# Optimization experiments

Measured on AMD Instinct MI355X. Metric: run time of the kernel, lower is better.

## Reference

```python
import jax, jax.numpy as jnp
import numpy as np

N_NODES = 100000
N_EDGES = 1600000
D_IN = 64
D_HID = 64
D_MLP = 32
D_OUT = 1


def setup_inputs() -> dict:
    key = jax.random.key(0)
    ks = jax.random.split(key, 12)
    s_in = 1.0 / np.sqrt(D_IN)
    s_h = 1.0 / np.sqrt(D_HID)
    s_m = 1.0 / np.sqrt(D_MLP)
    return {
        "x": jax.random.normal(ks[0], (N_NODES, D_IN), dtype=jnp.float32),
        "edge_index": jax.random.randint(ks[1], (2, N_EDGES), 0, N_NODES, dtype=jnp.int32),
        # SAGEConv 1: lin_l (aggregated neighbors, with bias), lin_r (root, no bias)
        "W1l": jax.random.normal(ks[2], (D_IN, D_HID), dtype=jnp.float32) * s_in,
        "b1l": jnp.zeros((D_HID,), dtype=jnp.float32),
        "W1r": jax.random.normal(ks[3], (D_IN, D_HID), dtype=jnp.float32) * s_in,
        # SAGEConv 2
        "W2l": jax.random.normal(ks[4], (D_HID, D_HID), dtype=jnp.float32) * s_h,
        "b2l": jnp.zeros((D_HID,), dtype=jnp.float32),
        "W2r": jax.random.normal(ks[5], (D_HID, D_HID), dtype=jnp.float32) * s_h,
        # MLP head
        "Wf1": jax.random.normal(ks[6], (D_HID, D_MLP), dtype=jnp.float32) * s_h,
        "bf1": jnp.zeros((D_MLP,), dtype=jnp.float32),
        "Wf2": jax.random.normal(ks[7], (D_MLP, D_OUT), dtype=jnp.float32) * s_m,
        "bf2": jnp.zeros((D_OUT,), dtype=jnp.float32),
    }


def _sage_conv(h, src, dst, Wl, bl, Wr):
    # mean-aggregate neighbor features (messages flow src -> dst)
    n = h.shape[0]
    agg = jax.ops.segment_sum(h[src], dst, num_segments=n)  # [N, D]
    cnt = jax.ops.segment_sum(jnp.ones((src.shape[0], 1), h.dtype), dst, num_segments=n)
    mean = agg / jnp.maximum(cnt, 1.0)  # isolated nodes -> 0
    return mean @ Wl + bl + h @ Wr


def reference(x, edge_index, W1l, b1l, W1r, W2l, b2l, W2r, Wf1, bf1, Wf2, bf2):
    src, dst = edge_index[0], edge_index[1]
    h = jax.nn.relu(_sage_conv(x, src, dst, W1l, b1l, W1r))
    h = jax.nn.relu(_sage_conv(h, src, dst, W2l, b2l, W2r))
    h = jax.nn.relu(h @ Wf1 + bf1)
    return jax.nn.sigmoid(h @ Wf2 + bf2)  # [N, 1]
```

## Files before the change

kernel.cpp:

```cpp
#include <hip/hip_runtime.h>
#include <math.h>

#define NN 100000
#define NE 1600000
#define D 64
#define DM 32
#define BK 128
#define NBUCK ((NN + BK - 1) / BK)
#define CAP 2560
#define MS_CHUNK 4096
#define N_MS ((NE + MS_CHUNK - 1) / MS_CHUNK)
#define NTILE ((NN + 63) / 64)

typedef unsigned int uint32;
typedef unsigned short ushort16;
typedef __attribute__((ext_vector_type(8))) short short8v;
typedef __attribute__((ext_vector_type(4))) float float4v;
typedef __attribute__((ext_vector_type(4))) uint32 uint4v;

__device__ __forceinline__ ushort16 f2bf(float f) {
    unsigned u = __float_as_uint(f);
    unsigned r = (u + 0x7FFF + ((u >> 16) & 1)) >> 16;
    return (ushort16)r;
}
__device__ __forceinline__ float bfLo(uint32 u) { return __uint_as_float(u << 16); }
__device__ __forceinline__ float bfHi(uint32 u) { return __uint_as_float(u & 0xFFFF0000u); }

__global__ __launch_bounds__(256) void prep_kernel(
    const float4* __restrict__ xin, ushort4* __restrict__ xoutb, int n4,
    const float* __restrict__ W1l, const float* __restrict__ W1r,
    const float* __restrict__ W2l, const float* __restrict__ W2r,
    const float* __restrict__ Wf1,
    ushort16* __restrict__ bfragL1, ushort16* __restrict__ bfragL2,
    ushort16* __restrict__ b2frag,
    int* __restrict__ bucketCursor)
{
    int b = blockIdx.x;
    if (b < 1024) {
        for (int i = b * 256 + threadIdx.x; i < n4; i += 1024 * 256) {
            float4 v = xin[i];
            ushort4 o;
            o.x = f2bf(v.x); o.y = f2bf(v.y); o.z = f2bf(v.z); o.w = f2bf(v.w);
            xoutb[i] = o;
        }
    } else if (b < 1056) {
        int tid = (b - 1024) * 256 + threadIdx.x;
        {
            int idx = tid;
            int i = idx & 7, l = (idx >> 3) & 63, jt = (idx >> 9) & 3, kb = idx >> 11;
            int k = kb * 32 + (l >> 4) * 8 + i;
            int j = jt * 16 + (l & 15);
            float v1 = (k < 64) ? W1l[k * 64 + j] : W1r[(k - 64) * 64 + j];
            float v2 = (k < 64) ? W2l[k * 64 + j] : W2r[(k - 64) * 64 + j];
            bfragL1[idx] = f2bf(v1);
            bfragL2[idx] = f2bf(v2);
        }
        if (tid < 2048) {
            int idx = tid;
            int i = idx & 7, l = (idx >> 3) & 63, jt2 = (idx >> 9) & 1, kb2 = idx >> 10;
            int k = kb2 * 32 + (l >> 4) * 8 + i;
            int j = jt2 * 16 + (l & 15);
            b2frag[idx] = f2bf(Wf1[k * 32 + j]);
        }
    } else {
        for (int t = threadIdx.x; t < NBUCK; t += 256)
            bucketCursor[t] = t * CAP;
    }
}

__global__ __launch_bounds__(1024) void multisplit_kernel(
    const int* __restrict__ src, const int* __restrict__ dst,
    int* __restrict__ bucketCursor, uint32* __restrict__ edgesPacked)
{
    __shared__ int lh[NBUCK];
    __shared__ int lbase[NBUCK];
    int t = threadIdx.x;
    if (t < NBUCK) lh[t] = 0;
    __syncthreads();
    int base = blockIdx.x * MS_CHUNK;
#pragma unroll
    for (int i = 0; i < MS_CHUNK / 1024; ++i) {
        int e = base + i * 1024 + t;
        if (e < NE) atomicAdd(&lh[dst[e] >> 7], 1);
    }
    __syncthreads();
    if (t < NBUCK) {
        int c = lh[t];
        lbase[t] = c ? atomicAdd(&bucketCursor[t], c) : 0;
        lh[t] = 0;
    }
    __syncthreads();
#pragma unroll
    for (int i = 0; i < MS_CHUNK / 1024; ++i) {
        int e = base + i * 1024 + t;
        if (e < NE) {
            int d = dst[e];
            int b = d >> 7;
            int r = atomicAdd(&lh[b], 1);
            edgesPacked[lbase[b] + r] = ((uint32)src[e] << 7) | (uint32)(d & 127);
        }
    }
}

__global__ __launch_bounds__(256) void reorder_csr_kernel(
    const uint32* __restrict__ edgesPacked,
    const int* __restrict__ bucketEnd,
    int* __restrict__ rowBeg, int* __restrict__ deg,
    int* __restrict__ sortedSrc)
{
    __shared__ int lcnt[BK];
    __shared__ int sc[BK];
    __shared__ int rowBegL[BK];
    int t = threadIdx.x;
    int b = blockIdx.x;
    int eBeg = b * CAP, eEnd = bucketEnd[b];

    if (t < BK) lcnt[t] = 0;
    __syncthreads();
    for (int e = eBeg + t; e < eEnd; e += 256)
        atomicAdd(&lcnt[edgesPacked[e] & 127], 1);
    __syncthreads();

    int myCnt = (t < BK) ? lcnt[t] : 0;
    if (t < BK) sc[t] = myCnt;
    __syncthreads();
#pragma unroll
    for (int off = 1; off < BK; off <<= 1) {
        int v = 0;
        if (t < BK && t >= off) v = sc[t - off];
        __syncthreads();
        if (t < BK) sc[t] += v;
        __syncthreads();
    }
    if (t < BK) {
        int excl = sc[t] - myCnt;
        int begHere = eBeg + excl;
        rowBegL[t] = begHere;
        int node = b * BK + t;
        if (node < NN) {
            rowBeg[node] = begHere;
            deg[node] = myCnt;
        }
        lcnt[t] = 0;
    }
    __syncthreads();

    for (int e = eBeg + t; e < eEnd; e += 256) {
        uint32 u = edgesPacked[e];
        int rel = (int)(u & 127);
        int rank = atomicAdd(&lcnt[rel], 1);
        sortedSrc[rowBegL[rel] + rank] = (int)(u >> 7);
    }
}

__global__ __launch_bounds__(256) void gather_mean_kernel(
    const uint2* __restrict__ hb2,
    const int* __restrict__ rowBeg, const int* __restrict__ deg,
    const int* __restrict__ ss,
    uint2* __restrict__ meanb2,
    int n)
{
    int lane = threadIdx.x & 63;
    int wid = threadIdx.x >> 6;
    int q = lane & 15;
    int g = lane >> 4;

    for (int node = blockIdx.x * 4 + wid; node < n; node += gridDim.x * 4) {
        int dg = deg[node];
        const int* ep = ss + rowBeg[node];
        float a0 = 0.f, a1 = 0.f, a2 = 0.f, a3 = 0.f;
        int nq = dg >> 2;
        int i = 0;
        for (; i + 4 <= nq; i += 4) {
            int s0 = ep[(i + 0) * 4 + g];
            int s1 = ep[(i + 1) * 4 + g];
            int s2 = ep[(i + 2) * 4 + g];
            int s3 = ep[(i + 3) * 4 + g];
            uint2 u0 = hb2[(size_t)s0 * 16 + q];
            uint2 u1 = hb2[(size_t)s1 * 16 + q];
            uint2 u2 = hb2[(size_t)s2 * 16 + q];
            uint2 u3 = hb2[(size_t)s3 * 16 + q];
            a0 += (bfLo(u0.x) + bfLo(u1.x)) + (bfLo(u2.x) + bfLo(u3.x));
            a1 += (bfHi(u0.x) + bfHi(u1.x)) + (bfHi(u2.x) + bfHi(u3.x));
            a2 += (bfLo(u0.y) + bfLo(u1.y)) + (bfLo(u2.y) + bfLo(u3.y));
            a3 += (bfHi(u0.y) + bfHi(u1.y)) + (bfHi(u2.y) + bfHi(u3.y));
        }
        for (; i < nq; ++i) {
            int s = ep[i * 4 + g];
            uint2 u = hb2[(size_t)s * 16 + q];
            a0 += bfLo(u.x); a1 += bfHi(u.x);
            a2 += bfLo(u.y); a3 += bfHi(u.y);
        }
        int rem = dg & 3;
        if (rem && g < rem) {
            int s = ep[nq * 4 + g];
            uint2 u = hb2[(size_t)s * 16 + q];
            a0 += bfLo(u.x); a1 += bfHi(u.x);
            a2 += bfLo(u.y); a3 += bfHi(u.y);
        }
        a0 += __shfl_xor(a0, 16); a0 += __shfl_xor(a0, 32);
        a1 += __shfl_xor(a1, 16); a1 += __shfl_xor(a1, 32);
        a2 += __shfl_xor(a2, 16); a2 += __shfl_xor(a2, 32);
        a3 += __shfl_xor(a3, 16); a3 += __shfl_xor(a3, 32);
        if (lane < 16) {
            float inv = (dg > 0) ? 1.0f / (float)dg : 0.0f;
            uint2 o;
            o.x = (uint32)f2bf(a0 * inv) | ((uint32)f2bf(a1 * inv) << 16);
            o.y = (uint32)f2bf(a2 * inv) | ((uint32)f2bf(a3 * inv) << 16);
            meanb2[(size_t)node * 16 + q] = o;
        }
    }
}

template <int WITH_MLP>
__global__ __launch_bounds__(256) void sage_mfma_kernel(
    const ushort16* __restrict__ rootb,
    const uint32* __restrict__ meanb32,
    const ushort16* __restrict__ bfrag,
    const ushort16* __restrict__ b2frag,
    const float* __restrict__ bl,
    const float* __restrict__ bf1, const float* __restrict__ Wf2,
    const float* __restrict__ bf2,
    ushort16* __restrict__ houtb,
    float* __restrict__ outp,
    int n)
{
    __shared__ ushort16 h2L[WITH_MLP ? (64 * 64) : 1];

    int lane = threadIdx.x & 63;
    int w = threadIdx.x >> 6;
    int c = lane & 15;
    int g = lane >> 4;
    int blkBase = blockIdx.x * 64;

    int arow = blkBase + w * 16 + c;
    bool aval = (arow < n);
    uint4v zero4 = {0u, 0u, 0u, 0u};
    const uint32* mrow = meanb32 + (size_t)arow * 32;
    const uint32* xrow = (const uint32*)rootb + (size_t)arow * 32;
    uint4v am0 = aval ? *(const uint4v*)(mrow + g * 4) : zero4;
    uint4v am1 = aval ? *(const uint4v*)(mrow + 16 + g * 4) : zero4;
    uint4v ax0 = aval ? *(const uint4v*)(xrow + g * 4) : zero4;
    uint4v ax1 = aval ? *(const uint4v*)(xrow + 16 + g * 4) : zero4;
    short8v a0 = __builtin_bit_cast(short8v, am0);
    short8v a1 = __builtin_bit_cast(short8v, am1);
    short8v a2 = __builtin_bit_cast(short8v, ax0);
    short8v a3 = __builtin_bit_cast(short8v, ax1);

    const short8v* bf = (const short8v*)bfrag;
    float4v acc[4];
#pragma unroll
    for (int jt = 0; jt < 4; ++jt) acc[jt] = (float4v){0.f, 0.f, 0.f, 0.f};
#pragma unroll
    for (int jt = 0; jt < 4; ++jt) {
        acc[jt] = __builtin_amdgcn_mfma_f32_16x16x32_bf16(a0, bf[(0 * 4 + jt) * 64 + lane], acc[jt], 0, 0, 0);
        acc[jt] = __builtin_amdgcn_mfma_f32_16x16x32_bf16(a1, bf[(1 * 4 + jt) * 64 + lane], acc[jt], 0, 0, 0);
        acc[jt] = __builtin_amdgcn_mfma_f32_16x16x32_bf16(a2, bf[(2 * 4 + jt) * 64 + lane], acc[jt], 0, 0, 0);
        acc[jt] = __builtin_amdgcn_mfma_f32_16x16x32_bf16(a3, bf[(3 * 4 + jt) * 64 + lane], acc[jt], 0, 0, 0);
    }

    float blv[4];
#pragma unroll
    for (int jt = 0; jt < 4; ++jt) blv[jt] = bl[jt * 16 + c];

    if (!WITH_MLP) {
#pragma unroll
        for (int jt = 0; jt < 4; ++jt) {
#pragma unroll
            for (int r = 0; r < 4; ++r) {
                int nd = blkBase + w * 16 + g * 4 + r;
                if (nd < n)
                    houtb[(size_t)nd * 64 + jt * 16 + c] =
                        f2bf(fmaxf(acc[jt][r] + blv[jt], 0.0f));
            }
        }
    } else {
#pragma unroll
        for (int jt = 0; jt < 4; ++jt) {
            int j = jt * 16 + c;
#pragma unroll
            for (int r = 0; r < 4; ++r) {
                int row = w * 16 + g * 4 + r;
                ushort16 hv = f2bf(fmaxf(acc[jt][r] + blv[jt], 0.0f));
                h2L[row * 64 + (((j >> 3) ^ (row & 7)) << 3) + (j & 7)] = hv;
            }
        }
        __syncthreads();

        int arow2 = w * 16 + c;
        short8v a2f[2];
#pragma unroll
        for (int kb2 = 0; kb2 < 2; ++kb2) {
            int chunk = (kb2 * 4 + g) ^ (arow2 & 7);
            a2f[kb2] = *(const short8v*)&h2L[arow2 * 64 + chunk * 8];
        }
        const short8v* b2f = (const short8v*)b2frag;
        float4v acc2[2];
#pragma unroll
        for (int jt2 = 0; jt2 < 2; ++jt2) acc2[jt2] = (float4v){0.f, 0.f, 0.f, 0.f};
#pragma unroll
        for (int jt2 = 0; jt2 < 2; ++jt2) {
            acc2[jt2] = __builtin_amdgcn_mfma_f32_16x16x32_bf16(a2f[0], b2f[(0 * 2 + jt2) * 64 + lane], acc2[jt2], 0, 0, 0);
            acc2[jt2] = __builtin_amdgcn_mfma_f32_16x16x32_bf16(a2f[1], b2f[(1 * 2 + jt2) * 64 + lane], acc2[jt2], 0, 0, 0);
        }

        float bf1v[2], f2v[2];
#pragma unroll
        for (int jt2 = 0; jt2 < 2; ++jt2) {
            bf1v[jt2] = bf1[jt2 * 16 + c];
            f2v[jt2]  = Wf2[jt2 * 16 + c];
        }
        float bias2 = bf2[0];

        float pv[4];
#pragma unroll
        for (int r = 0; r < 4; ++r) {
            float t = 0.0f;
#pragma unroll
            for (int jt2 = 0; jt2 < 2; ++jt2) {
                float h3 = fmaxf(acc2[jt2][r] + bf1v[jt2], 0.0f);
                t += h3 * f2v[jt2];
            }
#pragma unroll
            for (int off = 1; off <= 8; off <<= 1) t += __shfl_xor(t, off);
            pv[r] = t;
        }
        if (c == 0) {
#pragma unroll
            for (int r = 0; r < 4; ++r) {
                int nd = blkBase + w * 16 + g * 4 + r;
                if (nd < n)
                    outp[nd] = 1.0f / (1.0f + expf(-(pv[r] + bias2)));
            }
        }
    }
}

extern "C" void kernel_launch(void* const* d_in, const int* in_sizes, int n_in,
                              void* d_out, int out_size, void* d_ws, size_t ws_size,
                              hipStream_t stream)
{
    const float* x   = (const float*)d_in[0];
    const int*   ei  = (const int*)d_in[1];
    const float* W1l = (const float*)d_in[2];
    const float* b1l = (const float*)d_in[3];
    const float* W1r = (const float*)d_in[4];
    const float* W2l = (const float*)d_in[5];
    const float* b2l = (const float*)d_in[6];
    const float* W2r = (const float*)d_in[7];
    const float* Wf1 = (const float*)d_in[8];
    const float* bf1 = (const float*)d_in[9];
    const float* Wf2 = (const float*)d_in[10];
    const float* bf2 = (const float*)d_in[11];
    float* out = (float*)d_out;

    const int* src = ei;
    const int* dst = ei + NE;

    char* ws = (char*)d_ws;
    size_t off = 0;
    auto alloc = [&](size_t bytes) {
        char* p = ws + off;
        off = (off + bytes + 255) & ~(size_t)255;
        return p;
    };
    int* bucketCursor = (int*)alloc((size_t)NBUCK * sizeof(int));
    int* rowBeg       = (int*)alloc((size_t)NN * sizeof(int));
    int* deg          = (int*)alloc((size_t)NN * sizeof(int));
    uint32* edgesPacked = (uint32*)alloc((size_t)NBUCK * CAP * sizeof(uint32));
    int* sortedSrc      = (int*)alloc((size_t)NBUCK * CAP * sizeof(int));
    ushort16* xb    = (ushort16*)alloc((size_t)NN * D * sizeof(ushort16));
    ushort16* h1b   = (ushort16*)alloc((size_t)NN * D * sizeof(ushort16));
    uint32*   meanb = (uint32*)alloc((size_t)NN * (D / 2) * sizeof(uint32));
    ushort16* bfragL1 = (ushort16*)alloc(8192 * sizeof(ushort16));
    ushort16* bfragL2 = (ushort16*)alloc(8192 * sizeof(ushort16));
    ushort16* b2frag  = (ushort16*)alloc(2048 * sizeof(ushort16));

    dim3 blk(256);

    prep_kernel<<<1057, blk, 0, stream>>>(
        (const float4*)x, (ushort4*)xb, NN * D / 4,
        W1l, W1r, W2l, W2r, Wf1, bfragL1, bfragL2, b2frag, bucketCursor);

    multisplit_kernel<<<N_MS, dim3(1024), 0, stream>>>(src, dst, bucketCursor, edgesPacked);
    reorder_csr_kernel<<<NBUCK, blk, 0, stream>>>(
        edgesPacked, bucketCursor, rowBeg, deg, sortedSrc);

    gather_mean_kernel<<<2048, blk, 0, stream>>>(
        (const uint2*)xb, rowBeg, deg, sortedSrc, (uint2*)meanb, NN);
    sage_mfma_kernel<0><<<NTILE, blk, 0, stream>>>(
        xb, meanb, bfragL1, b2frag, b1l, bf1, Wf2, bf2, h1b, nullptr, NN);

    gather_mean_kernel<<<2048, blk, 0, stream>>>(
        (const uint2*)h1b, rowBeg, deg, sortedSrc, (uint2*)meanb, NN);
    sage_mfma_kernel<1><<<NTILE, blk, 0, stream>>>(
        h1b, meanb, bfragL2, b2frag, b2l, bf1, Wf2, bf2, nullptr, out, NN);
}
```

Baseline: 147.1 us.

## Widen CSR buckets to 512 nodes and use packed float2 accumulation in gather

Raises the bucket size of the two-pass CSR build from 128 to 512 destination nodes. This cuts the bucket count, so there are fewer global cursor atomics in the multisplit and fewer reorder blocks, each now 512 threads wide. The gather-mean kernel switches to float2 vector accumulators so the compiler can emit packed FP32 adds. Larger buckets raise per-bucket capacity needs (CAP 8960) and give less reorder parallelism. The packed adds also change the summation order slightly.

```diff
diff --git a/kernel.cpp b/kernel.cpp
--- a/kernel.cpp
+++ b/kernel.cpp
@@ -5,9 +5,10 @@
 #define NE 1600000
 #define D 64
 #define DM 32
-#define BK 128
+#define BK 512
 #define NBUCK ((NN + BK - 1) / BK)
-#define CAP 2560
+#define RELBITS 9
+#define CAP 8960
 #define MS_CHUNK 4096
 #define N_MS ((NE + MS_CHUNK - 1) / MS_CHUNK)
 #define NTILE ((NN + 63) / 64)
@@ -16,6 +17,7 @@
 typedef unsigned short ushort16;
 typedef __attribute__((ext_vector_type(8))) short short8v;
 typedef __attribute__((ext_vector_type(4))) float float4v;
+typedef __attribute__((ext_vector_type(2))) float float2v;
 typedef __attribute__((ext_vector_type(4))) uint32 uint4v;
 
 __device__ __forceinline__ ushort16 f2bf(float f) {
@@ -25,6 +27,12 @@
 }
 __device__ __forceinline__ float bfLo(uint32 u) { return __uint_as_float(u << 16); }
 __device__ __forceinline__ float bfHi(uint32 u) { return __uint_as_float(u & 0xFFFF0000u); }
+__device__ __forceinline__ float2v cvt2(uint32 u) {
+    float2v r;
+    r.x = bfLo(u);
+    r.y = bfHi(u);
+    return r;
+}
 
 __global__ __launch_bounds__(256) void prep_kernel(
     const float4* __restrict__ xin, ushort4* __restrict__ xoutb, int n4,
@@ -81,7 +89,7 @@
 #pragma unroll
     for (int i = 0; i < MS_CHUNK / 1024; ++i) {
         int e = base + i * 1024 + t;
-        if (e < NE) atomicAdd(&lh[dst[e] >> 7], 1);
+        if (e < NE) atomicAdd(&lh[dst[e] >> RELBITS], 1);
     }
     __syncthreads();
     if (t < NBUCK) {
@@ -95,14 +103,15 @@
         int e = base + i * 1024 + t;
         if (e < NE) {
             int d = dst[e];
-            int b = d >> 7;
+            int b = d >> RELBITS;
             int r = atomicAdd(&lh[b], 1);
-            edgesPacked[lbase[b] + r] = ((uint32)src[e] << 7) | (uint32)(d & 127);
-        }
-    }
-}
-
-__global__ __launch_bounds__(256) void reorder_csr_kernel(
+            edgesPacked[lbase[b] + r] =
+                ((uint32)src[e] << RELBITS) | (uint32)(d & (BK - 1));
+        }
+    }
+}
+
+__global__ __launch_bounds__(512) void reorder_csr_kernel(
     const uint32* __restrict__ edgesPacked,
     const int* __restrict__ bucketEnd,
     int* __restrict__ rowBeg, int* __restrict__ deg,
@@ -115,24 +124,23 @@
     int b = blockIdx.x;
     int eBeg = b * CAP, eEnd = bucketEnd[b];
 
-    if (t < BK) lcnt[t] = 0;
-    __syncthreads();
-    for (int e = eBeg + t; e < eEnd; e += 256)
-        atomicAdd(&lcnt[edgesPacked[e] & 127], 1);
-    __syncthreads();
-
-    int myCnt = (t < BK) ? lcnt[t] : 0;
-    if (t < BK) sc[t] = myCnt;
+    lcnt[t] = 0;
+    __syncthreads();
+    for (int e = eBeg + t; e < eEnd; e += 512)
+        atomicAdd(&lcnt[edgesPacked[e] & (BK - 1)], 1);
+    __syncthreads();
+
+    int myCnt = lcnt[t];
+    sc[t] = myCnt;
     __syncthreads();
 #pragma unroll
     for (int off = 1; off < BK; off <<= 1) {
-        int v = 0;
-        if (t < BK && t >= off) v = sc[t - off];
+        int v = (t >= off) ? sc[t - off] : 0;
         __syncthreads();
-        if (t < BK) sc[t] += v;
+        sc[t] += v;
         __syncthreads();
     }
-    if (t < BK) {
+    {
         int excl = sc[t] - myCnt;
         int begHere = eBeg + excl;
         rowBegL[t] = begHere;
@@ -145,11 +153,11 @@
     }
     __syncthreads();
 
-    for (int e = eBeg + t; e < eEnd; e += 256) {
+    for (int e = eBeg + t; e < eEnd; e += 512) {
         uint32 u = edgesPacked[e];
-        int rel = (int)(u & 127);
+        int rel = (int)(u & (BK - 1));
         int rank = atomicAdd(&lcnt[rel], 1);
-        sortedSrc[rowBegL[rel] + rank] = (int)(u >> 7);
+        sortedSrc[rowBegL[rel] + rank] = (int)(u >> RELBITS);
     }
 }
 
@@ -168,7 +176,8 @@
     for (int node = blockIdx.x * 4 + wid; node < n; node += gridDim.x * 4) {
         int dg = deg[node];
         const int* ep = ss + rowBeg[node];
-        float a0 = 0.f, a1 = 0.f, a2 = 0.f, a3 = 0.f;
+        float2v acc01 = {0.f, 0.f};
+        float2v acc23 = {0.f, 0.f};
         int nq = dg >> 2;
         int i = 0;
         for (; i + 4 <= nq; i += 4) {
@@ -180,24 +189,25 @@
             uint2 u1 = hb2[(size_t)s1 * 16 + q];
             uint2 u2 = hb2[(size_t)s2 * 16 + q];
             uint2 u3 = hb2[(size_t)s3 * 16 + q];
-            a0 += (bfLo(u0.x) + bfLo(u1.x)) + (bfLo(u2.x) + bfLo(u3.x));
-            a1 += (bfHi(u0.x) + bfHi(u1.x)) + (bfHi(u2.x) + bfHi(u3.x));
-            a2 += (bfLo(u0.y) + bfLo(u1.y)) + (bfLo(u2.y) + bfLo(u3.y));
-            a3 += (bfHi(u0.y) + bfHi(u1.y)) + (bfHi(u2.y) + bfHi(u3.y));
+            acc01 += cvt2(u0.x) + cvt2(u1.x);
+            acc23 += cvt2(u0.y) + cvt2(u1.y);
+            acc01 += cvt2(u2.x) + cvt2(u3.x);
+            acc23 += cvt2(u2.y) + cvt2(u3.y);
         }
         for (; i < nq; ++i) {
             int s = ep[i * 4 + g];
             uint2 u = hb2[(size_t)s * 16 + q];
-            a0 += bfLo(u.x); a1 += bfHi(u.x);
-            a2 += bfLo(u.y); a3 += bfHi(u.y);
+            acc01 += cvt2(u.x);
+            acc23 += cvt2(u.y);
         }
         int rem = dg & 3;
         if (rem && g < rem) {
             int s = ep[nq * 4 + g];
             uint2 u = hb2[(size_t)s * 16 + q];
-            a0 += bfLo(u.x); a1 += bfHi(u.x);
-            a2 += bfLo(u.y); a3 += bfHi(u.y);
-        }
+            acc01 += cvt2(u.x);
+            acc23 += cvt2(u.y);
+        }
+        float a0 = acc01.x, a1 = acc01.y, a2 = acc23.x, a3 = acc23.y;
         a0 += __shfl_xor(a0, 16); a0 += __shfl_xor(a0, 32);
         a1 += __shfl_xor(a1, 16); a1 += __shfl_xor(a1, 32);
         a2 += __shfl_xor(a2, 16); a2 += __shfl_xor(a2, 32);
@@ -383,7 +393,7 @@
         W1l, W1r, W2l, W2r, Wf1, bfragL1, bfragL2, b2frag, bucketCursor);
 
     multisplit_kernel<<<N_MS, dim3(1024), 0, stream>>>(src, dst, bucketCursor, edgesPacked);
-    reorder_csr_kernel<<<NBUCK, blk, 0, stream>>>(
+    reorder_csr_kernel<<<NBUCK, dim3(512), 0, stream>>>(
         edgesPacked, bucketCursor, rowBeg, deg, sortedSrc);
 
     gather_mean_kernel<<<2048, blk, 0, stream>>>(
```

Measured after the change: 147.8 us. Within noise of the previous version (+0.4%).
